# Kernel tuning notes

Hardware: AMD Instinct MI355X
Metric: run time of the kernel (lower is better)

Reference implementation:

```python
import jax, jax.numpy as jnp
import numpy as np

D_MODEL = 1024
NUM_HEADS = 16
LN_EPS = 1e-5


def setup_inputs() -> dict:
    key = jax.random.key(0)
    ks = jax.random.split(key, 7)
    B, S, D = 8, 1024, D_MODEL
    x = jax.random.normal(ks[0], (B, S, D), dtype=jnp.float32)
    # LayerNorm params (torch defaults: weight=1, bias=0; randomize slightly)
    ln_gamma = jnp.ones((D,), jnp.float32) + 0.02 * jax.random.normal(ks[1], (D,), jnp.float32)
    ln_beta = 0.02 * jax.random.normal(ks[2], (D,), jnp.float32)
    # nn.MultiheadAttention params: packed in_proj [3D, D], out_proj [D, D]
    scale = 1.0 / np.sqrt(D)
    in_proj_w = scale * jax.random.normal(ks[3], (3 * D, D), dtype=jnp.float32)
    in_proj_b = jnp.zeros((3 * D,), jnp.float32)
    out_proj_w = scale * jax.random.normal(ks[4], (D, D), dtype=jnp.float32)
    out_proj_b = jnp.zeros((D,), jnp.float32)
    return {
        "x": x,
        "ln_gamma": ln_gamma,
        "ln_beta": ln_beta,
        "in_proj_w": in_proj_w,
        "in_proj_b": in_proj_b,
        "out_proj_w": out_proj_w,
        "out_proj_b": out_proj_b,
    }


def reference(x, ln_gamma, ln_beta, in_proj_w, in_proj_b, out_proj_w, out_proj_b):
    B, S, D = x.shape
    H = NUM_HEADS
    Dh = D // H

    residual = x
    # LayerNorm (torch eps=1e-5)
    mu = jnp.mean(x, axis=-1, keepdims=True)
    var = jnp.mean(jnp.square(x - mu), axis=-1, keepdims=True)
    xn = (x - mu) * jax.lax.rsqrt(var + LN_EPS) * ln_gamma + ln_beta

    # Packed QKV projection: y = xn @ in_proj_w.T + in_proj_b
    qkv = jnp.einsum("bsd,ed->bse", xn, in_proj_w) + in_proj_b  # [B,S,3D]
    q, k, v = jnp.split(qkv, 3, axis=-1)

    def heads(t):  # [B,S,D] -> [B,H,S,Dh]
        return t.reshape(B, S, H, Dh).transpose(0, 2, 1, 3)

    q, k, v = heads(q), heads(k), heads(v)

    scores = jnp.einsum("bhsd,bhtd->bhst", q, k) / np.sqrt(Dh)  # [B,H,S,S]
    probs = jax.nn.softmax(scores, axis=-1)
    ctx = jnp.einsum("bhst,bhtd->bhsd", probs, v)  # [B,H,S,Dh]
    ctx = ctx.transpose(0, 2, 1, 3).reshape(B, S, D)

    attn_out = jnp.einsum("bsd,ed->bse", ctx, out_proj_w) + out_proj_b
    # (need_weights=True would also expose probs.mean over heads; math above
    #  matches the explicit non-flash path torch falls back to)
    return attn_out + residual
```

## Files before the change

### kernel.cpp

```cpp
#include <hip/hip_runtime.h>
#include <hip/hip_bf16.h>

typedef __bf16 bf16;
typedef __bf16 bf16x8 __attribute__((ext_vector_type(8)));
typedef __bf16 bf16x4 __attribute__((ext_vector_type(4)));
typedef float  f32x4  __attribute__((ext_vector_type(4)));

#define D_MODEL 1024
#define S_LEN   1024
#define NHEAD   16
#define DH      64

#define AS1 __attribute__((address_space(1)))
#define AS3 __attribute__((address_space(3)))

__global__ void cvt_kernel(const float* __restrict__ w1, bf16* __restrict__ o1, int n1,
                           const float* __restrict__ w2, bf16* __restrict__ o2, int n2) {
    int i = blockIdx.x * blockDim.x + threadIdx.x;
    const int stride = gridDim.x * blockDim.x;
    for (; i < n1 + n2; i += stride) {
        const float4 v = (i < n1) ? ((const float4*)w1)[i] : ((const float4*)w2)[i - n1];
        bf16x4 r;
        r[0] = (bf16)v.x; r[1] = (bf16)v.y; r[2] = (bf16)v.z; r[3] = (bf16)v.w;
        if (i < n1) ((bf16x4*)o1)[i] = r; else ((bf16x4*)o2)[i - n1] = r;
    }
}

__global__ __launch_bounds__(256) void ln_kernel(const float* __restrict__ x,
        const float* __restrict__ gamma, const float* __restrict__ beta,
        bf16* __restrict__ xn) {
    const int row = blockIdx.x;
    const int tid = threadIdx.x;
    const float4 v = ((const float4*)(x + (size_t)row * D_MODEL))[tid];
    float s  = v.x + v.y + v.z + v.w;
    float s2 = v.x*v.x + v.y*v.y + v.z*v.z + v.w*v.w;
    #pragma unroll
    for (int d = 1; d < 64; d <<= 1) { s += __shfl_xor(s, d); s2 += __shfl_xor(s2, d); }
    __shared__ float red[8];
    const int wave = tid >> 6;
    if ((tid & 63) == 0) { red[wave] = s; red[4 + wave] = s2; }
    __syncthreads();
    s  = red[0] + red[1] + red[2] + red[3];
    s2 = red[4] + red[5] + red[6] + red[7];
    const float mu   = s * (1.0f / D_MODEL);
    const float var  = s2 * (1.0f / D_MODEL) - mu * mu;
    const float rstd = rsqrtf(var + 1e-5f);
    const float4 g = ((const float4*)gamma)[tid];
    const float4 b = ((const float4*)beta)[tid];
    bf16x4 o;
    o[0] = (bf16)((v.x - mu) * rstd * g.x + b.x);
    o[1] = (bf16)((v.y - mu) * rstd * g.y + b.y);
    o[2] = (bf16)((v.z - mu) * rstd * g.z + b.z);
    o[3] = (bf16)((v.w - mu) * rstd * g.w + b.w);
    ((bf16x4*)(xn + (size_t)row * D_MODEL))[tid] = o;
}

#define GEMM_MAIN_LOOP(Ab, Wb, K)                                                        \
    f32x4 acc[4][4] = {};                                                                \
    for (int kt = 0; kt < (K); kt += 64) {                                               \
        _Pragma("unroll")                                                                \
        for (int i = 0; i < 4; ++i) {                                                    \
            const int L = i * 256 + tid;                                                 \
            const int r = L >> 3, blk = L & 7;                                           \
            const int src = (blk ^ (r & 7)) * 8;                                         \
            __builtin_amdgcn_global_load_lds(                                            \
                (const AS1 void*)((Ab) + (size_t)r * (K) + kt + src),                    \
                (AS3 void*)(As + L * 8), 16, 0, 0);                                      \
            __builtin_amdgcn_global_load_lds(                                            \
                (const AS1 void*)((Wb) + (size_t)r * (K) + kt + src),                    \
                (AS3 void*)(Bs + L * 8), 16, 0, 0);                                      \
        }                                                                                \
        __syncthreads();                                                                 \
        _Pragma("unroll")                                                                \
        for (int kk = 0; kk < 2; ++kk) {                                                 \
            bf16x8 af[4], bfm[4];                                                        \
            _Pragma("unroll")                                                            \
            for (int m = 0; m < 4; ++m) {                                                \
                const int R = wr * 64 + m * 16 + (lane & 15);                            \
                af[m] = *(const bf16x8*)(As + R * 64 +                                   \
                            (((kk * 4 + (lane >> 4)) ^ (R & 7)) << 3));                  \
            }                                                                            \
            _Pragma("unroll")                                                            \
            for (int n = 0; n < 4; ++n) {                                                \
                const int R = wc * 64 + n * 16 + (lane & 15);                            \
                bfm[n] = *(const bf16x8*)(Bs + R * 64 +                                  \
                            (((kk * 4 + (lane >> 4)) ^ (R & 7)) << 3));                  \
            }                                                                            \
            _Pragma("unroll")                                                            \
            for (int m = 0; m < 4; ++m)                                                  \
                _Pragma("unroll")                                                        \
                for (int n = 0; n < 4; ++n)                                              \
                    acc[m][n] = __builtin_amdgcn_mfma_f32_16x16x32_bf16(                 \
                        af[m], bfm[n], acc[m][n], 0, 0, 0);                              \
        }                                                                                \
        __syncthreads();                                                                 \
    }

#define XCD_REMAP()                                                                      \
    const int f = blockIdx.y * gridDim.x + blockIdx.x;                                   \
    const int xcd = f & 7;                                                               \
    const int rank = f >> 3;                                                             \
    const int brow = (xcd * 8 + (rank & 7)) * 128;                                       \
    const int bcol = (rank >> 3) * 128;

__global__ __launch_bounds__(256, 4) void gemm_qkv(
        const bf16* __restrict__ A, const bf16* __restrict__ W,
        const float* __restrict__ bias,
        bf16* __restrict__ q, bf16* __restrict__ k, bf16* __restrict__ vt) {
    __shared__ bf16 smem[2 * 128 * 64];
    bf16* As = smem;
    bf16* Bs = smem + 128 * 64;
    const int tid = threadIdx.x;
    const int lane = tid & 63;
    const int wave = tid >> 6;
    const int wr = wave >> 1, wc = wave & 1;
    XCD_REMAP()
    const bf16* Ab = A + (size_t)brow * 1024;
    const bf16* Wb = W + (size_t)bcol * 1024;

    GEMM_MAIN_LOOP(Ab, Wb, 1024)

    const int region = bcol >> 10;
    const int c = lane & 15, hh = lane >> 4;
    if (region == 2) {
        #pragma unroll
        for (int m = 0; m < 4; ++m) {
            #pragma unroll
            for (int n = 0; n < 4; ++n) {
                const int col = bcol + wc * 64 + n * 16 + c;
                const float bb = bias[col];
                const int e = col & 1023;
                const int h = e >> 6, dh = e & 63;
                const int row0 = brow + wr * 64 + m * 16 + hh * 4;
                const int b = row0 >> 10, s0 = row0 & 1023;
                const int bh = b * NHEAD + h;
                bf16x4 pk;
                #pragma unroll
                for (int j = 0; j < 4; ++j) pk[j] = (bf16)(acc[m][n][j] + bb);
                *(bf16x4*)(vt + ((size_t)bh * DH + dh) * S_LEN + s0) = pk;
            }
        }
    } else {
        const float qsc = (region == 0) ? 0.1803368801111244f : 1.0f;
        #pragma unroll
        for (int m = 0; m < 4; ++m) {
            #pragma unroll
            for (int n = 0; n < 4; ++n) {
                const int col = wc * 64 + n * 16 + c;
                const float bb = bias[bcol + col];
                #pragma unroll
                for (int j = 0; j < 4; ++j) {
                    const int row = wr * 64 + m * 16 + hh * 4 + j;
                    const int pb = (col >> 3) ^ (row & 7);
                    smem[row * 128 + pb * 8 + (col & 7)] = (bf16)((acc[m][n][j] + bb) * qsc);
                }
            }
        }
        __syncthreads();
        bf16* dst = (region == 0) ? q : k;
        #pragma unroll
        for (int i = 0; i < 8; ++i) {
            const int idx = i * 256 + tid;
            const int row = idx >> 4;
            const int bb = idx & 15;
            const bf16x8 vv = *(const bf16x8*)(smem + row * 128 + (bb ^ (row & 7)) * 8);
            const int grow = brow + row;
            const int s = grow & 1023, b = grow >> 10;
            const int col0 = bcol + bb * 8;
            const int e = col0 & 1023;
            const int h = e >> 6, dh = e & 63;
            *(bf16x8*)(dst + ((size_t)(b * NHEAD + h) * S_LEN + s) * DH + dh) = vv;
        }
    }
}

__global__ __launch_bounds__(256, 4) void gemm_out(
        const bf16* __restrict__ A, const bf16* __restrict__ W,
        const float* __restrict__ bias, const float* __restrict__ resid,
        float* __restrict__ out) {
    __shared__ bf16 smem[2 * 128 * 64];
    bf16* As = smem;
    bf16* Bs = smem + 128 * 64;
    const int tid = threadIdx.x;
    const int lane = tid & 63;
    const int wave = tid >> 6;
    const int wr = wave >> 1, wc = wave & 1;
    XCD_REMAP()
    const bf16* Ab = A + (size_t)brow * 1024;
    const bf16* Wb = W + (size_t)bcol * 1024;

    GEMM_MAIN_LOOP(Ab, Wb, 1024)

    #pragma unroll
    for (int m = 0; m < 4; ++m) {
        #pragma unroll
        for (int n = 0; n < 4; ++n) {
            const int col = bcol + wc * 64 + n * 16 + (lane & 15);
            const float bb = bias[col];
            #pragma unroll
            for (int j = 0; j < 4; ++j) {
                const int row = brow + wr * 64 + m * 16 + (lane >> 4) * 4 + j;
                const size_t idx = (size_t)row * D_MODEL + col;
                out[idx] = acc[m][n][j] + bb + resid[idx];
            }
        }
    }
}

__global__ __launch_bounds__(256, 4) void attn_kernel(
        const bf16* __restrict__ Q, const bf16* __restrict__ Kv,
        const bf16* __restrict__ Vt, bf16* __restrict__ ctx) {
    __shared__ bf16 KsB[2][64 * 64];
    __shared__ bf16 VsB[2][64 * 64];
    __shared__ bf16 PtB[4][32 * 64];
    const int tid = threadIdx.x;
    const int lane = tid & 63;
    const int w = tid >> 6;
    const int c = lane & 15;
    const int h = lane >> 4;
    const int bh = blockIdx.x;
    const int bb = bh >> 4, hd = bh & 15;
    const int q0 = blockIdx.y * 128 + w * 32;

    const bf16* Qh = Q + ((size_t)bh * S_LEN + q0) * DH;
    const char* Kb = (const char*)(Kv + (size_t)bh * S_LEN * DH);
    const char* Vb = (const char*)(Vt + (size_t)bh * DH * S_LEN);
    char* pw = (char*)&PtB[w][0];

    bf16x8 qf[2][2];
    #pragma unroll
    for (int nq = 0; nq < 2; ++nq)
        #pragma unroll
        for (int kk = 0; kk < 2; ++kk)
            qf[nq][kk] = *(const bf16x8*)(Qh + (16 * nq + c) * DH + kk * 32 + h * 8);

    f32x4 O[2][4] = {};
    float mr[2] = {-1e30f, -1e30f};
    float lr[2] = {0.0f, 0.0f};

#define STAGE(BB, KT) do {                                                               \
    _Pragma("unroll")                                                                    \
    for (int i = 0; i < 2; ++i) {                                                        \
        const int row = w * 16 + i * 8 + (lane >> 3);                                    \
        const int sw = ((lane & 7) ^ (row & 7)) << 4;                                    \
        const int lo = w * 2048 + i * 1024 + lane * 16;                                  \
        __builtin_amdgcn_global_load_lds(                                                \
            (const AS1 void*)(Kb + (size_t)((KT) + row) * 128 + sw),                     \
            (AS3 void*)((char*)&KsB[BB][0] + lo), 16, 0, 0);                             \
        __builtin_amdgcn_global_load_lds(                                                \
            (const AS1 void*)(Vb + (size_t)row * 2048 + (KT) * 2 + sw),                  \
            (AS3 void*)((char*)&VsB[BB][0] + lo), 16, 0, 0);                             \
    } } while (0)

    STAGE(0, 0);
    for (int t = 0; t < 16; ++t) {
        if (t < 15) {
            STAGE((t + 1) & 1, (t + 1) * 64);
            asm volatile("s_waitcnt vmcnt(4)" ::: "memory");
        } else {
            asm volatile("s_waitcnt vmcnt(0)" ::: "memory");
        }
        __builtin_amdgcn_s_barrier();
        const char* Ksb = (const char*)&KsB[t & 1][0];
        const char* Vsb = (const char*)&VsB[t & 1][0];

        f32x4 sf[2][4] = {};
        __builtin_amdgcn_s_setprio(1);
        #pragma unroll
        for (int kk = 0; kk < 2; ++kk) {
            bf16x8 kf[4];
            #pragma unroll
            for (int a = 0; a < 4; ++a)
                kf[a] = *(const bf16x8*)(Ksb + (16 * a + c) * 128 +
                                         (((4 * kk + h) ^ (c & 7)) << 4));
            #pragma unroll
            for (int nq = 0; nq < 2; ++nq)
                #pragma unroll
                for (int a = 0; a < 4; ++a)
                    sf[nq][a] = __builtin_amdgcn_mfma_f32_16x16x32_bf16(
                        kf[a], qf[nq][kk], sf[nq][a], 0, 0, 0);
        }
        __builtin_amdgcn_s_setprio(0);

        float resc[2];
        #pragma unroll
        for (int nq = 0; nq < 2; ++nq) {
            float pm = sf[nq][0][0];
            #pragma unroll
            for (int a = 0; a < 4; ++a)
                #pragma unroll
                for (int r = 0; r < 4; ++r)
                    pm = fmaxf(pm, sf[nq][a][r]);
            pm = fmaxf(pm, __shfl_xor(pm, 16));
            pm = fmaxf(pm, __shfl_xor(pm, 32));
            const float mn = fmaxf(mr[nq], pm);
            resc[nq] = __builtin_amdgcn_exp2f(mr[nq] - mn);
            mr[nq] = mn;
            float sum = 0.0f;
            #pragma unroll
            for (int a = 0; a < 4; ++a) {
                bf16x4 pk;
                #pragma unroll
                for (int r = 0; r < 4; ++r) {
                    const float p = __builtin_amdgcn_exp2f(sf[nq][a][r] - mn);
                    sum += p;
                    pk[r] = (bf16)p;
                }
                *(bf16x4*)(pw + (16 * nq + c) * 128 +
                           (((2 * a + (h >> 1)) ^ (c & 7)) << 4) + 8 * (h & 1)) = pk;
            }
            sum += __shfl_xor(sum, 16);
            sum += __shfl_xor(sum, 32);
            lr[nq] = lr[nq] * resc[nq] + sum;
        }

        #pragma unroll
        for (int mq = 0; mq < 2; ++mq) {
            float rs[4];
            #pragma unroll
            for (int r = 0; r < 4; ++r) rs[r] = __shfl(resc[mq], 4 * h + r);
            #pragma unroll
            for (int f2 = 0; f2 < 4; ++f2)
                #pragma unroll
                for (int r = 0; r < 4; ++r)
                    O[mq][f2][r] *= rs[r];
        }

        __builtin_amdgcn_s_setprio(1);
        #pragma unroll
        for (int kk = 0; kk < 2; ++kk) {
            bf16x8 pf[2], vf[4];
            #pragma unroll
            for (int mq = 0; mq < 2; ++mq)
                pf[mq] = *(const bf16x8*)(pw + (16 * mq + c) * 128 +
                                          (((4 * kk + h) ^ (c & 7)) << 4));
            #pragma unroll
            for (int f2 = 0; f2 < 4; ++f2)
                vf[f2] = *(const bf16x8*)(Vsb + (16 * f2 + c) * 128 +
                                          (((4 * kk + h) ^ (c & 7)) << 4));
            #pragma unroll
            for (int mq = 0; mq < 2; ++mq)
                #pragma unroll
                for (int f2 = 0; f2 < 4; ++f2)
                    O[mq][f2] = __builtin_amdgcn_mfma_f32_16x16x32_bf16(
                        pf[mq], vf[f2], O[mq][f2], 0, 0, 0);
        }
        __builtin_amdgcn_s_setprio(0);
        asm volatile("s_waitcnt lgkmcnt(0)" ::: "memory");
        __builtin_amdgcn_s_barrier();
    }
#undef STAGE

    const float invl0 = 1.0f / lr[0];
    const float invl1 = 1.0f / lr[1];
    #pragma unroll
    for (int mq = 0; mq < 2; ++mq) {
        float iv[4];
        #pragma unroll
        for (int r = 0; r < 4; ++r)
            iv[r] = __shfl(mq == 0 ? invl0 : invl1, 4 * h + r);
        #pragma unroll
        for (int f2 = 0; f2 < 4; ++f2)
            #pragma unroll
            for (int r = 0; r < 4; ++r) {
                const int s = q0 + 16 * mq + 4 * h + r;
                ctx[((size_t)(bb * S_LEN + s)) * D_MODEL + hd * DH + 16 * f2 + c] =
                    (bf16)(O[mq][f2][r] * iv[r]);
            }
    }
}

extern "C" void kernel_launch(void* const* d_in, const int* in_sizes, int n_in,
                              void* d_out, int out_size, void* d_ws, size_t ws_size,
                              hipStream_t stream) {
    const float* x     = (const float*)d_in[0];
    const float* gamma = (const float*)d_in[1];
    const float* beta  = (const float*)d_in[2];
    const float* in_w  = (const float*)d_in[3];
    const float* in_b  = (const float*)d_in[4];
    const float* out_w = (const float*)d_in[5];
    const float* out_b = (const float*)d_in[6];
    float* out = (float*)d_out;

    char* ws = (char*)d_ws;
    bf16* wq  = (bf16*)(ws);
    bf16* wo  = (bf16*)(ws + 6291456);
    bf16* xn  = (bf16*)(ws + 8388608);
    bf16* q   = (bf16*)(ws + 25165824);
    bf16* kk  = (bf16*)(ws + 41943040);
    bf16* vt  = (bf16*)(ws + 58720256);
    bf16* ctx = xn;

    hipLaunchKernelGGL(cvt_kernel, dim3(512), dim3(256), 0, stream,
                       in_w, wq, 3072 * 1024 / 4, out_w, wo, 1024 * 1024 / 4);
    hipLaunchKernelGGL(ln_kernel, dim3(8192), dim3(256), 0, stream, x, gamma, beta, xn);
    hipLaunchKernelGGL(gemm_qkv, dim3(64, 24), dim3(256), 0, stream, xn, wq, in_b, q, kk, vt);
    hipLaunchKernelGGL(attn_kernel, dim3(128, 8), dim3(256), 0, stream, q, kk, vt, ctx);
    hipLaunchKernelGGL(gemm_out, dim3(64, 8), dim3(256), 0, stream, ctx, wo, out_b, x, out);
}
```

Baseline: 170.1 us.

## Load K/V fragments directly from global memory and skip small softmax rescales

Removes the LDS double-buffered K/V staging and its block barriers; each wave now loads K and V MFMA fragments straight from global memory into registers. Adds a lazy online-softmax rescale that updates the running max and rescales O only when the new max exceeds the old by more than 8 (log2 units). Occupancy hint drops from 4 to 3 blocks per CU to allow more registers. The intent is to remove synchronisation and LDS traffic, at the cost of redundant global/L2 reads across the four waves and possibly unswizzled, less coalesced loads.

```diff
diff --git a/kernel.cpp b/kernel.cpp
--- a/kernel.cpp
+++ b/kernel.cpp
@@ -207,11 +207,9 @@
     }
 }
 
-__global__ __launch_bounds__(256, 4) void attn_kernel(
+__global__ __launch_bounds__(256, 3) void attn_kernel(
         const bf16* __restrict__ Q, const bf16* __restrict__ Kv,
         const bf16* __restrict__ Vt, bf16* __restrict__ ctx) {
-    __shared__ bf16 KsB[2][64 * 64];
-    __shared__ bf16 VsB[2][64 * 64];
     __shared__ bf16 PtB[4][32 * 64];
     const int tid = threadIdx.x;
     const int lane = tid & 63;
@@ -238,51 +236,35 @@
     float mr[2] = {-1e30f, -1e30f};
     float lr[2] = {0.0f, 0.0f};
 
-#define STAGE(BB, KT) do {                                                               \
-    _Pragma("unroll")                                                                    \
-    for (int i = 0; i < 2; ++i) {                                                        \
-        const int row = w * 16 + i * 8 + (lane >> 3);                                    \
-        const int sw = ((lane & 7) ^ (row & 7)) << 4;                                    \
-        const int lo = w * 2048 + i * 1024 + lane * 16;                                  \
-        __builtin_amdgcn_global_load_lds(                                                \
-            (const AS1 void*)(Kb + (size_t)((KT) + row) * 128 + sw),                     \
-            (AS3 void*)((char*)&KsB[BB][0] + lo), 16, 0, 0);                             \
-        __builtin_amdgcn_global_load_lds(                                                \
-            (const AS1 void*)(Vb + (size_t)row * 2048 + (KT) * 2 + sw),                  \
-            (AS3 void*)((char*)&VsB[BB][0] + lo), 16, 0, 0);                             \
-    } } while (0)
-
-    STAGE(0, 0);
-    for (int t = 0; t < 16; ++t) {
-        if (t < 15) {
-            STAGE((t + 1) & 1, (t + 1) * 64);
-            asm volatile("s_waitcnt vmcnt(4)" ::: "memory");
-        } else {
-            asm volatile("s_waitcnt vmcnt(0)" ::: "memory");
-        }
-        __builtin_amdgcn_s_barrier();
-        const char* Ksb = (const char*)&KsB[t & 1][0];
-        const char* Vsb = (const char*)&VsB[t & 1][0];
+    for (int kt = 0; kt < S_LEN; kt += 64) {
+        bf16x8 kf[2][4];
+        #pragma unroll
+        for (int kk = 0; kk < 2; ++kk)
+            #pragma unroll
+            for (int a = 0; a < 4; ++a)
+                kf[kk][a] = *(const bf16x8*)(Kb + (size_t)(kt + 16 * a + c) * 128 +
+                                             kk * 64 + h * 16);
 
         f32x4 sf[2][4] = {};
         __builtin_amdgcn_s_setprio(1);
         #pragma unroll
-        for (int kk = 0; kk < 2; ++kk) {
-            bf16x8 kf[4];
-            #pragma unroll
-            for (int a = 0; a < 4; ++a)
-                kf[a] = *(const bf16x8*)(Ksb + (16 * a + c) * 128 +
-                                         (((4 * kk + h) ^ (c & 7)) << 4));
+        for (int kk = 0; kk < 2; ++kk)
             #pragma unroll
             for (int nq = 0; nq < 2; ++nq)
                 #pragma unroll
                 for (int a = 0; a < 4; ++a)
                     sf[nq][a] = __builtin_amdgcn_mfma_f32_16x16x32_bf16(
-                        kf[a], qf[nq][kk], sf[nq][a], 0, 0, 0);
-        }
+                        kf[kk][a], qf[nq][kk], sf[nq][a], 0, 0, 0);
         __builtin_amdgcn_s_setprio(0);
 
-        float resc[2];
+        bf16x8 vf[2][4];
+        #pragma unroll
+        for (int kk = 0; kk < 2; ++kk)
+            #pragma unroll
+            for (int f2 = 0; f2 < 4; ++f2)
+                vf[kk][f2] = *(const bf16x8*)(Vb + (size_t)(16 * f2 + c) * 2048 +
+                                              (kt + kk * 32 + h * 8) * 2);
+
         #pragma unroll
         for (int nq = 0; nq < 2; ++nq) {
             float pm = sf[nq][0][0];
@@ -293,9 +275,21 @@
                     pm = fmaxf(pm, sf[nq][a][r]);
             pm = fmaxf(pm, __shfl_xor(pm, 16));
             pm = fmaxf(pm, __shfl_xor(pm, 32));
-            const float mn = fmaxf(mr[nq], pm);
-            resc[nq] = __builtin_amdgcn_exp2f(mr[nq] - mn);
-            mr[nq] = mn;
+            if (__any(pm > mr[nq] + 8.0f)) {
+                const float mn = fmaxf(mr[nq], pm);
+                const float rs = __builtin_amdgcn_exp2f(mr[nq] - mn);
+                mr[nq] = mn;
+                lr[nq] *= rs;
+                float rsr[4];
+                #pragma unroll
+                for (int r = 0; r < 4; ++r) rsr[r] = __shfl(rs, 4 * h + r);
+                #pragma unroll
+                for (int f2 = 0; f2 < 4; ++f2)
+                    #pragma unroll
+                    for (int r = 0; r < 4; ++r)
+                        O[nq][f2][r] *= rsr[r];
+            }
+            const float mn = mr[nq];
             float sum = 0.0f;
             #pragma unroll
             for (int a = 0; a < 4; ++a) {
@@ -311,45 +305,26 @@
             }
             sum += __shfl_xor(sum, 16);
             sum += __shfl_xor(sum, 32);
-            lr[nq] = lr[nq] * resc[nq] + sum;
-        }
-
-        #pragma unroll
-        for (int mq = 0; mq < 2; ++mq) {
-            float rs[4];
-            #pragma unroll
-            for (int r = 0; r < 4; ++r) rs[r] = __shfl(resc[mq], 4 * h + r);
-            #pragma unroll
-            for (int f2 = 0; f2 < 4; ++f2)
-                #pragma unroll
-                for (int r = 0; r < 4; ++r)
-                    O[mq][f2][r] *= rs[r];
+            lr[nq] += sum;
         }
 
         __builtin_amdgcn_s_setprio(1);
         #pragma unroll
         for (int kk = 0; kk < 2; ++kk) {
-            bf16x8 pf[2], vf[4];
+            bf16x8 pf[2];
             #pragma unroll
             for (int mq = 0; mq < 2; ++mq)
                 pf[mq] = *(const bf16x8*)(pw + (16 * mq + c) * 128 +
                                           (((4 * kk + h) ^ (c & 7)) << 4));
             #pragma unroll
-            for (int f2 = 0; f2 < 4; ++f2)
-                vf[f2] = *(const bf16x8*)(Vsb + (16 * f2 + c) * 128 +
-                                          (((4 * kk + h) ^ (c & 7)) << 4));
-            #pragma unroll
             for (int mq = 0; mq < 2; ++mq)
                 #pragma unroll
                 for (int f2 = 0; f2 < 4; ++f2)
                     O[mq][f2] = __builtin_amdgcn_mfma_f32_16x16x32_bf16(
-                        pf[mq], vf[f2], O[mq][f2], 0, 0, 0);
+                        pf[mq], vf[kk][f2], O[mq][f2], 0, 0, 0);
         }
         __builtin_amdgcn_s_setprio(0);
-        asm volatile("s_waitcnt lgkmcnt(0)" ::: "memory");
-        __builtin_amdgcn_s_barrier();
-    }
-#undef STAGE
+    }
 
     const float invl0 = 1.0f / lr[0];
     const float invl1 = 1.0f / lr[1];
```

New measurement: 222.7 us. +30.9%, slower.
